# Performance work log

Hardware: AMD Instinct MI355X
Metric: run time of the kernel (lower is better)

Reference implementation:

```python
import jax, jax.numpy as jnp
import numpy as np

NUM_HEADS = 8
ATTN_C = 8
EPS = 1e-5


def setup_inputs() -> dict:
    key = jax.random.key(0)
    ks = jax.random.split(key, 8)
    B, S, R, C = 1, 2048, 384, 64
    H, c = NUM_HEADS, ATTN_C
    sc = 1.0 / np.sqrt(C)
    return {
        "x1d": jax.random.normal(ks[0], (B, S, R, C), dtype=jnp.float32),
        "ln_w": jnp.ones((C,), jnp.float32),
        "ln_b": jnp.zeros((C,), jnp.float32),
        "Wq": jax.random.normal(ks[1], (C, H * c), jnp.float32) * sc,
        "Wk": jax.random.normal(ks[2], (C, c), jnp.float32) * sc,
        "Wv": jax.random.normal(ks[3], (C, c), jnp.float32) * sc,
        "Wg": jax.random.normal(ks[4], (C, H * c), jnp.float32) * sc,
        "bg": jnp.zeros((H * c,), jnp.float32),
        "Wf": jax.random.normal(ks[5], (H * c, C), jnpp := jnp.float32) * sc,
        "bf": jnp.zeros((C,), jnp.float32),
    }


def reference(x1d, ln_w, ln_b, Wq, Wk, Wv, Wg, bg, Wf, bf):
    H, c = NUM_HEADS, ATTN_C
    # swap seq/res axes: [B, S, R, C] -> [B, R, S, C]; attention runs over S (MSA column)
    x = jnp.swapaxes(x1d, -2, -3)
    mu = jnp.mean(x, axis=-1, keepdims=True)
    var = jnp.mean(jnp.square(x - mu), axis=-1, keepdims=True)
    xn = (x - mu) / jnp.sqrt(var + EPS) * ln_w + ln_b
    B, R, S, C = xn.shape
    # mean-pooled query over the sequence axis
    q_avg = jnp.mean(xn, axis=-2)                                  # [B, R, C]
    q = (q_avg @ Wq).reshape(B, R, H, c) * (c ** -0.5)             # [B, R, H, c]
    k = xn @ Wk                                                    # [B, R, S, c] (single shared head)
    v = xn @ Wv                                                    # [B, R, S, c]
    gate = jax.nn.sigmoid((xn @ Wg + bg).reshape(B, R, S, H, c))   # [B, R, S, H, c]
    w = jax.nn.softmax(jnp.einsum('brhc,brsc->brhs', q, k), axis=-1)  # [B, R, H, S]
    o = jnp.einsum('brhs,brsc->brhc', w, v)                        # [B, R, H, c]
    out = (o[:, :, None, :, :] * gate).reshape(B, R, S, H * c)     # broadcast over S, gated
    out = out @ Wf + bf                                            # [B, R, S, C]
    return jnp.swapaxes(out, -2, -3)                               # [B, S, R, C]
```

## Files before the change

kernel.cpp:

```cpp
#include <hip/hip_runtime.h>

#define SEQ  2048
#define RDIM 384
#define CDIM 64

typedef __attribute__((ext_vector_type(8))) short s16x8;
typedef __attribute__((ext_vector_type(4))) float f32x4;
#define MFMA(a,b,c) __builtin_amdgcn_mfma_f32_16x16x32_bf16(a,b,c,0,0,0)

__device__ __forceinline__ unsigned short f2bf(float x) {
    union { float f; unsigned u; } a; a.f = x;
    unsigned r = a.u + 0x7fffu + ((a.u >> 16) & 1u);
    return (unsigned short)(r >> 16);
}
__device__ __forceinline__ float bf2f(unsigned u16) {
    union { unsigned u; float f; } a; a.u = u16 << 16; return a.f;
}
__device__ __forceinline__ float sigmoidf_(float z) { return 1.0f / (1.0f + __expf(-z)); }

#define SWZ(row,k) ((row)*64 + (((((k)>>3) ^ ((row)&7)))<<3) + ((k)&7))

__global__ __launch_bounds__(256) void k_prep(
    const float* __restrict__ Wk, const float* __restrict__ Wv,
    const float* __restrict__ Wg, const float* __restrict__ Wf,
    unsigned short* __restrict__ wkvt, unsigned short* __restrict__ wgt,
    unsigned short* __restrict__ wfp)
{
    const int t = threadIdx.x, b = blockIdx.x;
    if (b == 0) {
        for (int idx = t; idx < 16 * 64; idx += 256) {
            const int kc = idx >> 6, k = idx & 63;
            const float v = (kc < 8) ? Wk[k * 8 + kc] : Wv[k * 8 + (kc - 8)];
            wkvt[SWZ(kc, k)] = f2bf(v);
        }
    } else if (b == 1) {
        for (int idx = t; idx < 64 * 64; idx += 256) {
            const int col = idx >> 6, k = idx & 63;
            wgt[SWZ(col, k)] = f2bf(Wg[k * 64 + col]);
        }
    } else {
        for (int idx = t; idx < 64 * 64; idx += 256) {
            const int cout = idx >> 6, p = idx & 63;
            const int kst = p >> 5, h = (p >> 3) & 3, rr = p & 7;
            const int j = kst * 32 + (rr < 4 ? 4 * h + rr : 16 + 4 * h + (rr - 4));
            wfp[SWZ(cout, p)] = f2bf(Wf[j * 64 + cout]);
        }
    }
}

__global__ __launch_bounds__(256) void k_phase1(
    const float* __restrict__ x, const float* __restrict__ lnw, const float* __restrict__ lnb,
    const unsigned short* __restrict__ wkvt,
    float* __restrict__ qpart, unsigned short* __restrict__ kv)
{
    __shared__ __align__(16) unsigned short xs[128 * 64];
    __shared__ __align__(16) unsigned short wkv[16 * 64];
    const int t = threadIdx.x;
    ((unsigned*)wkv)[t]       = ((const unsigned*)wkvt)[t];
    ((unsigned*)wkv)[t + 256] = ((const unsigned*)wkvt)[t + 256];

    const int rtile  = blockIdx.x % 24;
    const int schunk = blockIdx.x / 24;
    const int g  = t >> 4;
    const int c4 = t & 15;
    const int r  = rtile * 16 + g;
    const int wv = t >> 6, lane = t & 63, hi = lane >> 4, l15 = lane & 15;
    const float4 lw = *(const float4*)(lnw + (c4 << 2));
    const float4 lb = *(const float4*)(lnb + (c4 << 2));

    float qs0 = 0.f, qs1 = 0.f, qs2 = 0.f, qs3 = 0.f;
    for (int sub = 0; sub < 8; ++sub) {
        __syncthreads();
        #pragma unroll
        for (int it = 0; it < 8; ++it) {
            const int row = it * 16 + g;
            const int s = schunk * 64 + sub * 8 + it;
            const float4 xv = *(const float4*)(x + ((size_t)s * RDIM + r) * CDIM + (c4 << 2));
            float sum = xv.x + xv.y + xv.z + xv.w;
            float sq  = xv.x * xv.x + xv.y * xv.y + xv.z * xv.z + xv.w * xv.w;
            #pragma unroll
            for (int m = 1; m < 16; m <<= 1) {
                sum += __shfl_xor(sum, m, 16);
                sq  += __shfl_xor(sq,  m, 16);
            }
            const float mu   = sum * (1.0f / 64.0f);
            const float rstd = rsqrtf(sq * (1.0f / 64.0f) - mu * mu + 1e-5f);
            const float xn0 = (xv.x - mu) * rstd * lw.x + lb.x;
            const float xn1 = (xv.y - mu) * rstd * lw.y + lb.y;
            const float xn2 = (xv.z - mu) * rstd * lw.z + lb.z;
            const float xn3 = (xv.w - mu) * rstd * lw.w + lb.w;
            qs0 += xn0; qs1 += xn1; qs2 += xn2; qs3 += xn3;
            ushort4 pk; pk.x = f2bf(xn0); pk.y = f2bf(xn1); pk.z = f2bf(xn2); pk.w = f2bf(xn3);
            *(ushort4*)&xs[row * 64 + ((((c4 >> 1) ^ (row & 7)) << 3) | ((c4 & 1) << 2))] = pk;
        }
        __syncthreads();
        f32x4 acc0 = 0, acc1 = 0;
        #pragma unroll
        for (int kst = 0; kst < 2; ++kst) {
            const int kg = (kst * 4 + hi);
            const s16x8 a = *(const s16x8*)&wkv[l15 * 64 + ((kg ^ (l15 & 7)) << 3)];
            const int row0 = wv * 32 + l15;
            const s16x8 b0 = *(const s16x8*)&xs[row0 * 64 + ((kg ^ (l15 & 7)) << 3)];
            const s16x8 b1 = *(const s16x8*)&xs[(row0 + 16) * 64 + ((kg ^ (l15 & 7)) << 3)];
            acc0 = MFMA(a, b0, acc0);
            acc1 = MFMA(a, b1, acc1);
        }
        #pragma unroll
        for (int ni = 0; ni < 2; ++ni) {
            const f32x4 av = ni ? acc1 : acc0;
            const int srow = schunk * 64 + sub * 8 + 2 * wv + ni;
            const int rrow = rtile * 16 + l15;
            ushort4 pk; pk.x = f2bf(av[0]); pk.y = f2bf(av[1]); pk.z = f2bf(av[2]); pk.w = f2bf(av[3]);
            *(ushort4*)(kv + ((size_t)srow * RDIM + rrow) * 16 + (hi << 2)) = pk;
        }
    }
    float4 q4; q4.x = qs0; q4.y = qs1; q4.z = qs2; q4.w = qs3;
    *(float4*)(qpart + ((size_t)schunk * RDIM + r) * CDIM + (c4 << 2)) = q4;
}

__global__ __launch_bounds__(256) void k_phase2(
    const float* __restrict__ qpart, const float* __restrict__ Wq,
    const unsigned short* __restrict__ kv, float* __restrict__ obuf)
{
    __shared__ float qa[64];
    __shared__ float ql[64];
    __shared__ float hredm[4][8];
    __shared__ float hredd[4][8];
    __shared__ float maxs[8];
    __shared__ float dens[8];
    __shared__ float wred[4][64];
    const int t = threadIdx.x;
    const int r = (blockIdx.x & 7) * 48 + (blockIdx.x >> 3);
    if (t < 64) {
        float ssum = 0.f;
        #pragma unroll
        for (int ch = 0; ch < 32; ch++) ssum += qpart[(size_t)ch * (RDIM * CDIM) + r * 64 + t];
        qa[t] = ssum;
    }
    __syncthreads();
    if (t < 64) {
        float a = 0.f;
        for (int i = 0; i < 64; i++) a += qa[i] * Wq[i * 64 + t];
        ql[t] = a * (1.0f / 2048.0f) * 0.35355339059327373f;
    }
    __syncthreads();

    const unsigned short* kvr = kv + (size_t)r * 16;
    float l[8][8];
    #pragma unroll
    for (int i = 0; i < 8; i++) {
        const int s = t + i * 256;
        const uint4 ku = *(const uint4*)(kvr + (size_t)s * (RDIM * 16));
        float kf[8];
        kf[0] = bf2f(ku.x & 0xffff); kf[1] = bf2f(ku.x >> 16);
        kf[2] = bf2f(ku.y & 0xffff); kf[3] = bf2f(ku.y >> 16);
        kf[4] = bf2f(ku.z & 0xffff); kf[5] = bf2f(ku.z >> 16);
        kf[6] = bf2f(ku.w & 0xffff); kf[7] = bf2f(ku.w >> 16);
        #pragma unroll
        for (int h = 0; h < 8; h++) {
            float a = 0.f;
            #pragma unroll
            for (int c = 0; c < 8; c++) a += ql[h * 8 + c] * kf[c];
            l[i][h] = a;
        }
    }
    float pm[8];
    #pragma unroll
    for (int h = 0; h < 8; h++) {
        pm[h] = l[0][h];
        #pragma unroll
        for (int i = 1; i < 8; i++) pm[h] = fmaxf(pm[h], l[i][h]);
    }
    #pragma unroll
    for (int m = 1; m < 64; m <<= 1) {
        #pragma unroll
        for (int h = 0; h < 8; h++) pm[h] = fmaxf(pm[h], __shfl_xor(pm[h], m, 64));
    }
    const int wvi = t >> 6, lane = t & 63;
    if (lane == 0) {
        #pragma unroll
        for (int h = 0; h < 8; h++) hredm[wvi][h] = pm[h];
    }
    __syncthreads();
    if (t < 8) maxs[t] = fmaxf(fmaxf(hredm[0][t], hredm[1][t]), fmaxf(hredm[2][t], hredm[3][t]));
    __syncthreads();

    float pd[8] = {0,0,0,0,0,0,0,0};
    #pragma unroll
    for (int i = 0; i < 8; i++) {
        #pragma unroll
        for (int h = 0; h < 8; h++) {
            const float e = __expf(l[i][h] - maxs[h]);
            l[i][h] = e;
            pd[h] += e;
        }
    }
    #pragma unroll
    for (int m = 1; m < 64; m <<= 1) {
        #pragma unroll
        for (int h = 0; h < 8; h++) pd[h] += __shfl_xor(pd[h], m, 64);
    }
    if (lane == 0) {
        #pragma unroll
        for (int h = 0; h < 8; h++) hredd[wvi][h] = pd[h];
    }
    __syncthreads();
    if (t < 8) dens[t] = hredd[0][t] + hredd[1][t] + hredd[2][t] + hredd[3][t];

    float acc[64];
    #pragma unroll
    for (int j = 0; j < 64; j++) acc[j] = 0.f;
    #pragma unroll
    for (int i = 0; i < 8; i++) {
        const int s = t + i * 256;
        const uint4 vu = *(const uint4*)(kvr + (size_t)s * (RDIM * 16) + 8);
        float vf[8];
        vf[0] = bf2f(vu.x & 0xffff); vf[1] = bf2f(vu.x >> 16);
        vf[2] = bf2f(vu.y & 0xffff); vf[3] = bf2f(vu.y >> 16);
        vf[4] = bf2f(vu.z & 0xffff); vf[5] = bf2f(vu.z >> 16);
        vf[6] = bf2f(vu.w & 0xffff); vf[7] = bf2f(vu.w >> 16);
        #pragma unroll
        for (int h = 0; h < 8; h++) {
            const float w = l[i][h];
            #pragma unroll
            for (int c = 0; c < 8; c++) acc[h * 8 + c] += w * vf[c];
        }
    }
    #pragma unroll
    for (int m = 1; m < 64; m <<= 1) {
        #pragma unroll
        for (int j = 0; j < 64; j++) acc[j] += __shfl_xor(acc[j], m, 64);
    }
    if (lane == 0) {
        #pragma unroll
        for (int j = 0; j < 64; j++) wred[wvi][j] = acc[j];
    }
    __syncthreads();
    if (t < 64)
        obuf[(size_t)r * 64 + t] = (wred[0][t] + wred[1][t] + wred[2][t] + wred[3][t]) / dens[t >> 3];
}

__global__ __launch_bounds__(256) void k_phase3(
    const float* __restrict__ x, const float* __restrict__ lnw, const float* __restrict__ lnb,
    const unsigned short* __restrict__ wgt, const unsigned short* __restrict__ wfp,
    const float* __restrict__ bg, const float* __restrict__ bf_,
    const float* __restrict__ obuf, float* __restrict__ out)
{
    __shared__ __align__(16) unsigned short xs[128 * 64];
    __shared__ __align__(16) unsigned short wg[64 * 64];
    __shared__ __align__(16) unsigned short wf[64 * 64];
    __shared__ __align__(16) unsigned short olds[128 * 68];
    __shared__ __align__(16) float bgl[64];
    __shared__ __align__(16) float bfl[64];
    const int t = threadIdx.x;
    const int rtile = blockIdx.x % 3;
    const int sb    = blockIdx.x / 3;
    const int rbase = rtile * 128;

    #pragma unroll
    for (int i = 0; i < 8; ++i) ((unsigned*)wg)[t + i * 256] = ((const unsigned*)wgt)[t + i * 256];
    #pragma unroll
    for (int i = 0; i < 8; ++i) ((unsigned*)wf)[t + i * 256] = ((const unsigned*)wfp)[t + i * 256];
    if (t < 64) { bgl[t] = bg[t]; bfl[t] = bf_[t]; }
    #pragma unroll
    for (int i = 0; i < 8; ++i) {
        const int idx = t + i * 256;
        const int row = idx >> 4, c = idx & 15;
        const float4 ov = *(const float4*)(obuf + (size_t)(rbase + row) * 64 + (c << 2));
        ushort4 pk; pk.x = f2bf(ov.x); pk.y = f2bf(ov.y); pk.z = f2bf(ov.z); pk.w = f2bf(ov.w);
        *(ushort4*)&olds[row * 68 + (c << 2)] = pk;
    }

    const int g = t >> 4, c4 = t & 15;
    const float4 lw = *(const float4*)(lnw + (c4 << 2));
    const float4 lb = *(const float4*)(lnb + (c4 << 2));
    const int wv = t >> 6, lane = t & 63, hi = lane >> 4, l15 = lane & 15;
    float bfv[4];

    for (int si = 0; si < 4; ++si) {
        const int s = sb * 4 + si;
        __syncthreads();
        #pragma unroll
        for (int it = 0; it < 8; ++it) {
            const int row = it * 16 + g;
            const float4 xv = *(const float4*)(x + ((size_t)s * RDIM + rbase + row) * CDIM + (c4 << 2));
            float sum = xv.x + xv.y + xv.z + xv.w;
            float sq  = xv.x * xv.x + xv.y * xv.y + xv.z * xv.z + xv.w * xv.w;
            #pragma unroll
            for (int m = 1; m < 16; m <<= 1) {
                sum += __shfl_xor(sum, m, 16);
                sq  += __shfl_xor(sq,  m, 16);
            }
            const float mu   = sum * (1.0f / 64.0f);
            const float rstd = rsqrtf(sq * (1.0f / 64.0f) - mu * mu + 1e-5f);
            ushort4 pk;
            pk.x = f2bf((xv.x - mu) * rstd * lw.x + lb.x);
            pk.y = f2bf((xv.y - mu) * rstd * lw.y + lb.y);
            pk.z = f2bf((xv.z - mu) * rstd * lw.z + lb.z);
            pk.w = f2bf((xv.w - mu) * rstd * lw.w + lb.w);
            *(ushort4*)&xs[row * 64 + ((((c4 >> 1) ^ (row & 7)) << 3) | ((c4 & 1) << 2))] = pk;
        }
        __syncthreads();

        f32x4 acc1[4][2];
        #pragma unroll
        for (int mi = 0; mi < 4; ++mi) { acc1[mi][0] = 0; acc1[mi][1] = 0; }
        #pragma unroll
        for (int kst = 0; kst < 2; ++kst) {
            const int kg = kst * 4 + hi;
            s16x8 bfr[2];
            #pragma unroll
            for (int ni = 0; ni < 2; ++ni) {
                const int row = wv * 32 + ni * 16 + l15;
                bfr[ni] = *(const s16x8*)&xs[row * 64 + ((kg ^ (l15 & 7)) << 3)];
            }
            #pragma unroll
            for (int mi = 0; mi < 4; ++mi) {
                const int col = mi * 16 + l15;
                const s16x8 afr = *(const s16x8*)&wg[col * 64 + ((kg ^ (l15 & 7)) << 3)];
                acc1[mi][0] = MFMA(afr, bfr[0], acc1[mi][0]);
                acc1[mi][1] = MFMA(afr, bfr[1], acc1[mi][1]);
            }
        }

        s16x8 a2[2][2];
        #pragma unroll
        for (int ni = 0; ni < 2; ++ni) {
            const int row = wv * 32 + ni * 16 + l15;
            #pragma unroll
            for (int mi = 0; mi < 4; ++mi) {
                const int jb = mi * 16 + (hi << 2);
                const ushort4 ou = *(const ushort4*)&olds[row * 68 + jb];
                float o4[4];
                o4[0] = bf2f(ou.x); o4[1] = bf2f(ou.y); o4[2] = bf2f(ou.z); o4[3] = bf2f(ou.w);
                const f32x4 bg4 = *(const f32x4*)&bgl[jb];
                #pragma unroll
                for (int rg = 0; rg < 4; ++rg) {
                    const float z = acc1[mi][ni][rg] + bg4[rg];
                    const float tv = sigmoidf_(z) * o4[rg];
                    a2[ni][mi >> 1][((mi & 1) << 2) + rg] = (short)f2bf(tv);
                }
            }
        }

        f32x4 acc2[2][4];
        #pragma unroll
        for (int ni = 0; ni < 2; ++ni)
            #pragma unroll
            for (int ci = 0; ci < 4; ++ci) acc2[ni][ci] = 0;
        #pragma unroll
        for (int kst = 0; kst < 2; ++kst) {
            const int kg = kst * 4 + hi;
            #pragma unroll
            for (int ci = 0; ci < 4; ++ci) {
                const int co = ci * 16 + l15;
                const s16x8 bfr = *(const s16x8*)&wf[co * 64 + ((kg ^ (l15 & 7)) << 3)];
                acc2[0][ci] = MFMA(a2[0][kst], bfr, acc2[0][ci]);
                acc2[1][ci] = MFMA(a2[1][kst], bfr, acc2[1][ci]);
            }
        }

        #pragma unroll
        for (int ci = 0; ci < 4; ++ci) bfv[ci] = bfl[ci * 16 + l15];
        #pragma unroll
        for (int ni = 0; ni < 2; ++ni) {
            #pragma unroll
            for (int rg = 0; rg < 4; ++rg) {
                const int row = wv * 32 + ni * 16 + (hi << 2) + rg;
                float* op = out + ((size_t)s * RDIM + rbase + row) * CDIM + l15;
                #pragma unroll
                for (int ci = 0; ci < 4; ++ci)
                    op[ci * 16] = acc2[ni][ci][rg] + bfv[ci];
            }
        }
    }
}

extern "C" void kernel_launch(void* const* d_in, const int* in_sizes, int n_in,
                              void* d_out, int out_size, void* d_ws, size_t ws_size,
                              hipStream_t stream)
{
    const float* x   = (const float*)d_in[0];
    const float* lnw = (const float*)d_in[1];
    const float* lnb = (const float*)d_in[2];
    const float* Wq  = (const float*)d_in[3];
    const float* Wk  = (const float*)d_in[4];
    const float* Wv  = (const float*)d_in[5];
    const float* Wg  = (const float*)d_in[6];
    const float* bg  = (const float*)d_in[7];
    const float* Wf  = (const float*)d_in[8];
    const float* bf  = (const float*)d_in[9];

    char* ws = (char*)d_ws;
    float* qpart         = (float*)ws;
    float* obuf          = (float*)(ws + 3145728);
    unsigned short* kv   = (unsigned short*)(ws + 3244032);
    unsigned short* wkvt = (unsigned short*)(ws + 28409856);
    unsigned short* wgt  = wkvt + 1024;
    unsigned short* wfp  = wgt + 4096;

    float* outp = (float*)d_out;

    k_prep<<<3, 256, 0, stream>>>(Wk, Wv, Wg, Wf, wkvt, wgt, wfp);
    k_phase1<<<768, 256, 0, stream>>>(x, lnw, lnb, wkvt, qpart, kv);
    k_phase2<<<384, 256, 0, stream>>>(qpart, Wq, kv, obuf);
    k_phase3<<<1536, 256, 0, stream>>>(x, lnw, lnb, wgt, wfp, bg, bf, obuf, outp);
}
```

Baseline: 181.3 us.

## Fold LayerNorm affine into weights, split softmax phase, double-buffer gating kernel

Folds the LayerNorm scale and shift into the K/V, gate and query weights, with precomputed bias vectors, so the per-element affine work disappears from phase 1 and phase 3. Moves kv to a residue-major layout and rewrites phase 2 as a single-pass softmax without max subtraction, split over two sequence halves, plus a small combine kernel. That kernel also writes the attention output pre-swizzled into the phase 3 register fragment layout. Phase 3 processes 8 sequence rows per block with register prefetch of the next row, double-buffered LDS, float4 output stores and launch bounds for 3 blocks per CU. Dropping the max subtraction risks exp overflow if logits become large.

```diff
diff --git a/kernel.cpp b/kernel.cpp
--- a/kernel.cpp
+++ b/kernel.cpp
@@ -13,30 +13,49 @@
     unsigned r = a.u + 0x7fffu + ((a.u >> 16) & 1u);
     return (unsigned short)(r >> 16);
 }
+__device__ __forceinline__ unsigned pack2(float lo, float hi) {
+    return (unsigned)f2bf(lo) | ((unsigned)f2bf(hi) << 16);
+}
 __device__ __forceinline__ float bf2f(unsigned u16) {
     union { unsigned u; float f; } a; a.u = u16 << 16; return a.f;
 }
-__device__ __forceinline__ float sigmoidf_(float z) { return 1.0f / (1.0f + __expf(-z)); }
+__device__ __forceinline__ float uaf(unsigned u) {
+    union { unsigned u; float f; } a; a.u = u; return a.f;
+}
 
 #define SWZ(row,k) ((row)*64 + (((((k)>>3) ^ ((row)&7)))<<3) + ((k)&7))
 
 __global__ __launch_bounds__(256) void k_prep(
     const float* __restrict__ Wk, const float* __restrict__ Wv,
     const float* __restrict__ Wg, const float* __restrict__ Wf,
+    const float* __restrict__ lnw, const float* __restrict__ lnb,
+    const float* __restrict__ bg,
     unsigned short* __restrict__ wkvt, unsigned short* __restrict__ wgt,
-    unsigned short* __restrict__ wfp)
+    unsigned short* __restrict__ wfp, float* __restrict__ kvbias,
+    float* __restrict__ bgp)
 {
     const int t = threadIdx.x, b = blockIdx.x;
     if (b == 0) {
         for (int idx = t; idx < 16 * 64; idx += 256) {
             const int kc = idx >> 6, k = idx & 63;
-            const float v = (kc < 8) ? Wk[k * 8 + kc] : Wv[k * 8 + (kc - 8)];
+            const float v = lnw[k] * ((kc < 8) ? Wk[k * 8 + kc] : Wv[k * 8 + (kc - 8)]);
             wkvt[SWZ(kc, k)] = f2bf(v);
+        }
+        if (t < 16) {
+            float a = 0.f;
+            for (int k = 0; k < 64; k++)
+                a += lnb[k] * ((t < 8) ? Wk[k * 8 + t] : Wv[k * 8 + (t - 8)]);
+            kvbias[t] = a;
         }
     } else if (b == 1) {
         for (int idx = t; idx < 64 * 64; idx += 256) {
             const int col = idx >> 6, k = idx & 63;
-            wgt[SWZ(col, k)] = f2bf(Wg[k * 64 + col]);
+            wgt[SWZ(col, k)] = f2bf(lnw[k] * Wg[k * 64 + col]);
+        }
+        if (t < 64) {
+            float a = bg[t];
+            for (int k = 0; k < 64; k++) a += lnb[k] * Wg[k * 64 + t];
+            bgp[t] = a;
         }
     } else {
         for (int idx = t; idx < 64 * 64; idx += 256) {
@@ -49,8 +68,7 @@
 }
 
 __global__ __launch_bounds__(256) void k_phase1(
-    const float* __restrict__ x, const float* __restrict__ lnw, const float* __restrict__ lnb,
-    const unsigned short* __restrict__ wkvt,
+    const float* __restrict__ x, const unsigned short* __restrict__ wkvt,
     float* __restrict__ qpart, unsigned short* __restrict__ kv)
 {
     __shared__ __align__(16) unsigned short xs[128 * 64];
@@ -63,10 +81,8 @@
     const int schunk = blockIdx.x / 24;
     const int g  = t >> 4;
     const int c4 = t & 15;
-    const int r  = rtile * 16 + g;
+    const int r = rtile * 16 + g;
     const int wv = t >> 6, lane = t & 63, hi = lane >> 4, l15 = lane & 15;
-    const float4 lw = *(const float4*)(lnw + (c4 << 2));
-    const float4 lb = *(const float4*)(lnb + (c4 << 2));
 
     float qs0 = 0.f, qs1 = 0.f, qs2 = 0.f, qs3 = 0.f;
     for (int sub = 0; sub < 8; ++sub) {
@@ -85,10 +101,10 @@
             }
             const float mu   = sum * (1.0f / 64.0f);
             const float rstd = rsqrtf(sq * (1.0f / 64.0f) - mu * mu + 1e-5f);
-            const float xn0 = (xv.x - mu) * rstd * lw.x + lb.x;
-            const float xn1 = (xv.y - mu) * rstd * lw.y + lb.y;
-            const float xn2 = (xv.z - mu) * rstd * lw.z + lb.z;
-            const float xn3 = (xv.w - mu) * rstd * lw.w + lb.w;
+            const float xn0 = (xv.x - mu) * rstd;
+            const float xn1 = (xv.y - mu) * rstd;
+            const float xn2 = (xv.z - mu) * rstd;
+            const float xn3 = (xv.w - mu) * rstd;
             qs0 += xn0; qs1 += xn1; qs2 += xn2; qs3 += xn3;
             ushort4 pk; pk.x = f2bf(xn0); pk.y = f2bf(xn1); pk.z = f2bf(xn2); pk.w = f2bf(xn3);
             *(ushort4*)&xs[row * 64 + ((((c4 >> 1) ^ (row & 7)) << 3) | ((c4 & 1) << 2))] = pk;
@@ -111,26 +127,27 @@
             const int srow = schunk * 64 + sub * 8 + 2 * wv + ni;
             const int rrow = rtile * 16 + l15;
             ushort4 pk; pk.x = f2bf(av[0]); pk.y = f2bf(av[1]); pk.z = f2bf(av[2]); pk.w = f2bf(av[3]);
-            *(ushort4*)(kv + ((size_t)srow * RDIM + rrow) * 16 + (hi << 2)) = pk;
+            *(ushort4*)(kv + ((size_t)rrow * SEQ + srow) * 16 + (hi << 2)) = pk;
         }
     }
     float4 q4; q4.x = qs0; q4.y = qs1; q4.z = qs2; q4.w = qs3;
     *(float4*)(qpart + ((size_t)schunk * RDIM + r) * CDIM + (c4 << 2)) = q4;
 }
 
-__global__ __launch_bounds__(256) void k_phase2(
+__global__ __launch_bounds__(256) void k_phase2a(
     const float* __restrict__ qpart, const float* __restrict__ Wq,
-    const unsigned short* __restrict__ kv, float* __restrict__ obuf)
+    const float* __restrict__ lnw, const float* __restrict__ lnb,
+    const float* __restrict__ kvbias, const unsigned short* __restrict__ kv,
+    float* __restrict__ num, float* __restrict__ den)
 {
     __shared__ float qa[64];
     __shared__ float ql[64];
-    __shared__ float hredm[4][8];
+    __shared__ float lbias[8];
     __shared__ float hredd[4][8];
-    __shared__ float maxs[8];
-    __shared__ float dens[8];
     __shared__ float wred[4][64];
     const int t = threadIdx.x;
-    const int r = (blockIdx.x & 7) * 48 + (blockIdx.x >> 3);
+    const int r = blockIdx.x >> 1;
+    const int half = blockIdx.x & 1;
     if (t < 64) {
         float ssum = 0.f;
         #pragma unroll
@@ -140,209 +157,208 @@
     __syncthreads();
     if (t < 64) {
         float a = 0.f;
-        for (int i = 0; i < 64; i++) a += qa[i] * Wq[i * 64 + t];
-        ql[t] = a * (1.0f / 2048.0f) * 0.35355339059327373f;
+        for (int i = 0; i < 64; i++)
+            a += (qa[i] * (1.0f / 2048.0f) * lnw[i] + lnb[i]) * Wq[i * 64 + t];
+        ql[t] = a * 0.35355339059327373f;
     }
     __syncthreads();
-
-    const unsigned short* kvr = kv + (size_t)r * 16;
-    float l[8][8];
-    #pragma unroll
-    for (int i = 0; i < 8; i++) {
-        const int s = t + i * 256;
-        const uint4 ku = *(const uint4*)(kvr + (size_t)s * (RDIM * 16));
-        float kf[8];
+    if (t < 8) {
+        float a = 0.f;
+        #pragma unroll
+        for (int c = 0; c < 8; c++) a += ql[t * 8 + c] * kvbias[c];
+        lbias[t] = a;
+    }
+    __syncthreads();
+
+    const unsigned short* kvr = kv + (size_t)r * (SEQ * 16);
+    float acc[64];
+    float pd[8];
+    #pragma unroll
+    for (int j = 0; j < 64; j++) acc[j] = 0.f;
+    #pragma unroll
+    for (int h = 0; h < 8; h++) pd[h] = 0.f;
+
+    #pragma unroll
+    for (int i = 0; i < 4; i++) {
+        const int s = half * 1024 + i * 256 + t;
+        const uint4 ku = *(const uint4*)(kvr + (size_t)s * 16);
+        const uint4 vu = *(const uint4*)(kvr + (size_t)s * 16 + 8);
+        float kf[8], vf[8];
         kf[0] = bf2f(ku.x & 0xffff); kf[1] = bf2f(ku.x >> 16);
         kf[2] = bf2f(ku.y & 0xffff); kf[3] = bf2f(ku.y >> 16);
         kf[4] = bf2f(ku.z & 0xffff); kf[5] = bf2f(ku.z >> 16);
         kf[6] = bf2f(ku.w & 0xffff); kf[7] = bf2f(ku.w >> 16);
-        #pragma unroll
-        for (int h = 0; h < 8; h++) {
-            float a = 0.f;
-            #pragma unroll
-            for (int c = 0; c < 8; c++) a += ql[h * 8 + c] * kf[c];
-            l[i][h] = a;
-        }
-    }
-    float pm[8];
-    #pragma unroll
-    for (int h = 0; h < 8; h++) {
-        pm[h] = l[0][h];
-        #pragma unroll
-        for (int i = 1; i < 8; i++) pm[h] = fmaxf(pm[h], l[i][h]);
-    }
-    #pragma unroll
-    for (int m = 1; m < 64; m <<= 1) {
-        #pragma unroll
-        for (int h = 0; h < 8; h++) pm[h] = fmaxf(pm[h], __shfl_xor(pm[h], m, 64));
-    }
-    const int wvi = t >> 6, lane = t & 63;
-    if (lane == 0) {
-        #pragma unroll
-        for (int h = 0; h < 8; h++) hredm[wvi][h] = pm[h];
-    }
-    __syncthreads();
-    if (t < 8) maxs[t] = fmaxf(fmaxf(hredm[0][t], hredm[1][t]), fmaxf(hredm[2][t], hredm[3][t]));
-    __syncthreads();
-
-    float pd[8] = {0,0,0,0,0,0,0,0};
-    #pragma unroll
-    for (int i = 0; i < 8; i++) {
-        #pragma unroll
-        for (int h = 0; h < 8; h++) {
-            const float e = __expf(l[i][h] - maxs[h]);
-            l[i][h] = e;
-            pd[h] += e;
-        }
-    }
-    #pragma unroll
-    for (int m = 1; m < 64; m <<= 1) {
-        #pragma unroll
-        for (int h = 0; h < 8; h++) pd[h] += __shfl_xor(pd[h], m, 64);
-    }
-    if (lane == 0) {
-        #pragma unroll
-        for (int h = 0; h < 8; h++) hredd[wvi][h] = pd[h];
-    }
-    __syncthreads();
-    if (t < 8) dens[t] = hredd[0][t] + hredd[1][t] + hredd[2][t] + hredd[3][t];
-
-    float acc[64];
-    #pragma unroll
-    for (int j = 0; j < 64; j++) acc[j] = 0.f;
-    #pragma unroll
-    for (int i = 0; i < 8; i++) {
-        const int s = t + i * 256;
-        const uint4 vu = *(const uint4*)(kvr + (size_t)s * (RDIM * 16) + 8);
-        float vf[8];
         vf[0] = bf2f(vu.x & 0xffff); vf[1] = bf2f(vu.x >> 16);
         vf[2] = bf2f(vu.y & 0xffff); vf[3] = bf2f(vu.y >> 16);
         vf[4] = bf2f(vu.z & 0xffff); vf[5] = bf2f(vu.z >> 16);
         vf[6] = bf2f(vu.w & 0xffff); vf[7] = bf2f(vu.w >> 16);
         #pragma unroll
         for (int h = 0; h < 8; h++) {
-            const float w = l[i][h];
-            #pragma unroll
-            for (int c = 0; c < 8; c++) acc[h * 8 + c] += w * vf[c];
+            float a = lbias[h];
+            #pragma unroll
+            for (int c = 0; c < 8; c++) a += ql[h * 8 + c] * kf[c];
+            const float e = __expf(a);
+            pd[h] += e;
+            #pragma unroll
+            for (int c = 0; c < 8; c++) acc[h * 8 + c] += e * vf[c];
         }
     }
     #pragma unroll
     for (int m = 1; m < 64; m <<= 1) {
         #pragma unroll
         for (int j = 0; j < 64; j++) acc[j] += __shfl_xor(acc[j], m, 64);
-    }
+        #pragma unroll
+        for (int h = 0; h < 8; h++) pd[h] += __shfl_xor(pd[h], m, 64);
+    }
+    const int wvi = t >> 6, lane = t & 63;
     if (lane == 0) {
         #pragma unroll
         for (int j = 0; j < 64; j++) wred[wvi][j] = acc[j];
+        #pragma unroll
+        for (int h = 0; h < 8; h++) hredd[wvi][h] = pd[h];
     }
     __syncthreads();
     if (t < 64)
-        obuf[(size_t)r * 64 + t] = (wred[0][t] + wred[1][t] + wred[2][t] + wred[3][t]) / dens[t >> 3];
-}
-
-__global__ __launch_bounds__(256) void k_phase3(
-    const float* __restrict__ x, const float* __restrict__ lnw, const float* __restrict__ lnb,
+        num[(size_t)(half * RDIM + r) * 64 + t] = wred[0][t] + wred[1][t] + wred[2][t] + wred[3][t];
+    if (t < 8)
+        den[(size_t)(half * RDIM + r) * 8 + t] = hredd[0][t] + hredd[1][t] + hredd[2][t] + hredd[3][t];
+}
+
+__global__ __launch_bounds__(256) void k_phase2b(
+    const float* __restrict__ num, const float* __restrict__ den,
+    const float* __restrict__ kvbias, unsigned short* __restrict__ ofimg)
+{
+    const int idx = blockIdx.x * 256 + threadIdx.x;
+    const int r = idx >> 6, c = idx & 63;
+    const float n = num[idx] + num[RDIM * 64 + idx];
+    const float d = den[r * 8 + (c >> 3)] + den[(RDIM + r) * 8 + (c >> 3)];
+    const float o = n / d + kvbias[8 + (c & 7)];
+    const int rt = r >> 7, row = r & 127;
+    const int wv = row >> 5, ni = (row >> 4) & 1, l15 = row & 15;
+    const int mi = c >> 4, hi = (c >> 2) & 3, rg = c & 3;
+    const int tt = wv * 64 + hi * 16 + l15;
+    const int slot = ni * 16 + mi * 4 + rg;
+    ofimg[((rt * 256 + tt) << 5) + slot] = f2bf(o);
+}
+
+__global__ __launch_bounds__(256, 3) void k_phase3(
+    const float* __restrict__ x,
     const unsigned short* __restrict__ wgt, const unsigned short* __restrict__ wfp,
-    const float* __restrict__ bg, const float* __restrict__ bf_,
-    const float* __restrict__ obuf, float* __restrict__ out)
-{
-    __shared__ __align__(16) unsigned short xs[128 * 64];
+    const float* __restrict__ bgp, const float* __restrict__ bf_,
+    const unsigned short* __restrict__ ofimg, float* __restrict__ out)
+{
+    __shared__ __align__(16) unsigned short xs[2][128 * 64];
     __shared__ __align__(16) unsigned short wg[64 * 64];
     __shared__ __align__(16) unsigned short wf[64 * 64];
-    __shared__ __align__(16) unsigned short olds[128 * 68];
-    __shared__ __align__(16) float bgl[64];
-    __shared__ __align__(16) float bfl[64];
     const int t = threadIdx.x;
-    const int rtile = blockIdx.x % 3;
-    const int sb    = blockIdx.x / 3;
-    const int rbase = rtile * 128;
+    const int rt = blockIdx.x % 3;
+    const int sb = blockIdx.x / 3;
+    const int rbase = rt * 128;
 
     #pragma unroll
     for (int i = 0; i < 8; ++i) ((unsigned*)wg)[t + i * 256] = ((const unsigned*)wgt)[t + i * 256];
     #pragma unroll
     for (int i = 0; i < 8; ++i) ((unsigned*)wf)[t + i * 256] = ((const unsigned*)wfp)[t + i * 256];
-    if (t < 64) { bgl[t] = bg[t]; bfl[t] = bf_[t]; }
-    #pragma unroll
-    for (int i = 0; i < 8; ++i) {
-        const int idx = t + i * 256;
-        const int row = idx >> 4, c = idx & 15;
-        const float4 ov = *(const float4*)(obuf + (size_t)(rbase + row) * 64 + (c << 2));
-        ushort4 pk; pk.x = f2bf(ov.x); pk.y = f2bf(ov.y); pk.z = f2bf(ov.z); pk.w = f2bf(ov.w);
-        *(ushort4*)&olds[row * 68 + (c << 2)] = pk;
-    }
-
-    const int g = t >> 4, c4 = t & 15;
-    const float4 lw = *(const float4*)(lnw + (c4 << 2));
-    const float4 lb = *(const float4*)(lnb + (c4 << 2));
+
     const int wv = t >> 6, lane = t & 63, hi = lane >> 4, l15 = lane & 15;
-    float bfv[4];
-
-    for (int si = 0; si < 4; ++si) {
-        const int s = sb * 4 + si;
-        __syncthreads();
-        #pragma unroll
-        for (int it = 0; it < 8; ++it) {
-            const int row = it * 16 + g;
-            const float4 xv = *(const float4*)(x + ((size_t)s * RDIM + rbase + row) * CDIM + (c4 << 2));
-            float sum = xv.x + xv.y + xv.z + xv.w;
-            float sq  = xv.x * xv.x + xv.y * xv.y + xv.z * xv.z + xv.w * xv.w;
-            #pragma unroll
-            for (int m = 1; m < 16; m <<= 1) {
-                sum += __shfl_xor(sum, m, 16);
-                sq  += __shfl_xor(sq,  m, 16);
-            }
+
+    unsigned opk[16];
+    {
+        const unsigned* osrc = (const unsigned*)ofimg + (size_t)(rt * 256 + t) * 16;
+        #pragma unroll
+        for (int i = 0; i < 16; ++i) opk[i] = osrc[i];
+    }
+    float bgf[4][4], bff[4][4];
+    #pragma unroll
+    for (int mi = 0; mi < 4; ++mi) *(float4*)bgf[mi] = *(const float4*)(bgp + mi * 16 + hi * 4);
+    #pragma unroll
+    for (int ci = 0; ci < 4; ++ci) *(float4*)bff[ci] = *(const float4*)(bf_ + ci * 16 + hi * 4);
+
+    const int li = t & 3, p = t >> 2;
+    float4 xv[2][4];
+    {
+        const int s0 = sb * 8;
+        #pragma unroll
+        for (int k = 0; k < 2; ++k) {
+            const float* xp = x + ((size_t)s0 * RDIM + rbase + k * 64 + p) * CDIM + li * 16;
+            #pragma unroll
+            for (int j = 0; j < 4; ++j) xv[k][j] = *(const float4*)(xp + j * 4);
+        }
+    }
+
+    for (int si = 0; si < 8; ++si) {
+        const int s = sb * 8 + si;
+        unsigned short* xb = xs[si & 1];
+        #pragma unroll
+        for (int k = 0; k < 2; ++k) {
+            const int row = k * 64 + p;
+            float sum = 0.f, sq = 0.f;
+            #pragma unroll
+            for (int j = 0; j < 4; ++j) {
+                sum += xv[k][j].x + xv[k][j].y + xv[k][j].z + xv[k][j].w;
+                sq  += xv[k][j].x * xv[k][j].x + xv[k][j].y * xv[k][j].y
+                     + xv[k][j].z * xv[k][j].z + xv[k][j].w * xv[k][j].w;
+            }
+            sum += __shfl_xor(sum, 1, 4); sum += __shfl_xor(sum, 2, 4);
+            sq  += __shfl_xor(sq,  1, 4); sq  += __shfl_xor(sq,  2, 4);
             const float mu   = sum * (1.0f / 64.0f);
             const float rstd = rsqrtf(sq * (1.0f / 64.0f) - mu * mu + 1e-5f);
-            ushort4 pk;
-            pk.x = f2bf((xv.x - mu) * rstd * lw.x + lb.x);
-            pk.y = f2bf((xv.y - mu) * rstd * lw.y + lb.y);
-            pk.z = f2bf((xv.z - mu) * rstd * lw.z + lb.z);
-            pk.w = f2bf((xv.w - mu) * rstd * lw.w + lb.w);
-            *(ushort4*)&xs[row * 64 + ((((c4 >> 1) ^ (row & 7)) << 3) | ((c4 & 1) << 2))] = pk;
-        }
-        __syncthreads();
+            uint4 w0, w1;
+            w0.x = pack2((xv[k][0].x - mu) * rstd, (xv[k][0].y - mu) * rstd);
+            w0.y = pack2((xv[k][0].z - mu) * rstd, (xv[k][0].w - mu) * rstd);
+            w0.z = pack2((xv[k][1].x - mu) * rstd, (xv[k][1].y - mu) * rstd);
+            w0.w = pack2((xv[k][1].z - mu) * rstd, (xv[k][1].w - mu) * rstd);
+            w1.x = pack2((xv[k][2].x - mu) * rstd, (xv[k][2].y - mu) * rstd);
+            w1.y = pack2((xv[k][2].z - mu) * rstd, (xv[k][2].w - mu) * rstd);
+            w1.z = pack2((xv[k][3].x - mu) * rstd, (xv[k][3].y - mu) * rstd);
+            w1.w = pack2((xv[k][3].z - mu) * rstd, (xv[k][3].w - mu) * rstd);
+            *(uint4*)&xb[row * 64 + (((2 * li)     ^ (row & 7)) << 3)] = w0;
+            *(uint4*)&xb[row * 64 + (((2 * li + 1) ^ (row & 7)) << 3)] = w1;
+        }
+        if (si < 7) {
+            const int sn = s + 1;
+            #pragma unroll
+            for (int k = 0; k < 2; ++k) {
+                const float* xp = x + ((size_t)sn * RDIM + rbase + k * 64 + p) * CDIM + li * 16;
+                #pragma unroll
+                for (int j = 0; j < 4; ++j) xv[k][j] = *(const float4*)(xp + j * 4);
+            }
+        }
+        asm volatile("s_waitcnt lgkmcnt(0)" ::: "memory");
+        __builtin_amdgcn_s_barrier();
+        asm volatile("" ::: "memory");
 
         f32x4 acc1[4][2];
         #pragma unroll
         for (int mi = 0; mi < 4; ++mi) { acc1[mi][0] = 0; acc1[mi][1] = 0; }
         #pragma unroll
         for (int kst = 0; kst < 2; ++kst) {
-            const int kg = kst * 4 + hi;
-            s16x8 bfr[2];
-            #pragma unroll
-            for (int ni = 0; ni < 2; ++ni) {
-                const int row = wv * 32 + ni * 16 + l15;
-                bfr[ni] = *(const s16x8*)&xs[row * 64 + ((kg ^ (l15 & 7)) << 3)];
-            }
+            const int swz = (((kst * 4 + hi) ^ (l15 & 7)) << 3);
+            const s16x8 bfr0 = *(const s16x8*)&xb[(wv * 32 + l15) * 64 + swz];
+            const s16x8 bfr1 = *(const s16x8*)&xb[(wv * 32 + 16 + l15) * 64 + swz];
             #pragma unroll
             for (int mi = 0; mi < 4; ++mi) {
-                const int col = mi * 16 + l15;
-                const s16x8 afr = *(const s16x8*)&wg[col * 64 + ((kg ^ (l15 & 7)) << 3)];
-                acc1[mi][0] = MFMA(afr, bfr[0], acc1[mi][0]);
-                acc1[mi][1] = MFMA(afr, bfr[1], acc1[mi][1]);
-            }
-        }
-
+                const s16x8 afr = *(const s16x8*)&wg[(mi * 16 + l15) * 64 + swz];
+                acc1[mi][0] = MFMA(afr, bfr0, acc1[mi][0]);
+                acc1[mi][1] = MFMA(afr, bfr1, acc1[mi][1]);
+            }
+        }
         s16x8 a2[2][2];
         #pragma unroll
         for (int ni = 0; ni < 2; ++ni) {
-            const int row = wv * 32 + ni * 16 + l15;
             #pragma unroll
             for (int mi = 0; mi < 4; ++mi) {
-                const int jb = mi * 16 + (hi << 2);
-                const ushort4 ou = *(const ushort4*)&olds[row * 68 + jb];
-                float o4[4];
-                o4[0] = bf2f(ou.x); o4[1] = bf2f(ou.y); o4[2] = bf2f(ou.z); o4[3] = bf2f(ou.w);
-                const f32x4 bg4 = *(const f32x4*)&bgl[jb];
                 #pragma unroll
                 for (int rg = 0; rg < 4; ++rg) {
-                    const float z = acc1[mi][ni][rg] + bg4[rg];
-                    const float tv = sigmoidf_(z) * o4[rg];
+                    const int slot = ni * 16 + mi * 4 + rg;
+                    const unsigned u = opk[slot >> 1];
+                    const float of = uaf((slot & 1) ? (u & 0xffff0000u) : (u << 16));
+                    const float z = acc1[mi][ni][rg] + bgf[mi][rg];
+                    const float tv = of / (1.0f + __expf(-z));
                     a2[ni][mi >> 1][((mi & 1) << 2) + rg] = (short)f2bf(tv);
                 }
             }
         }
-
         f32x4 acc2[2][4];
         #pragma unroll
         for (int ni = 0; ni < 2; ++ni)
@@ -350,27 +366,25 @@
             for (int ci = 0; ci < 4; ++ci) acc2[ni][ci] = 0;
         #pragma unroll
         for (int kst = 0; kst < 2; ++kst) {
-            const int kg = kst * 4 + hi;
+            const int swz = (((kst * 4 + hi) ^ (l15 & 7)) << 3);
             #pragma unroll
             for (int ci = 0; ci < 4; ++ci) {
-                const int co = ci * 16 + l15;
-                const s16x8 bfr = *(const s16x8*)&wf[co * 64 + ((kg ^ (l15 & 7)) << 3)];
-                acc2[0][ci] = MFMA(a2[0][kst], bfr, acc2[0][ci]);
-                acc2[1][ci] = MFMA(a2[1][kst], bfr, acc2[1][ci]);
-            }
-        }
-
-        #pragma unroll
-        for (int ci = 0; ci < 4; ++ci) bfv[ci] = bfl[ci * 16 + l15];
+                const s16x8 wffr = *(const s16x8*)&wf[(ci * 16 + l15) * 64 + swz];
+                acc2[0][ci] = MFMA(wffr, a2[0][kst], acc2[0][ci]);
+                acc2[1][ci] = MFMA(wffr, a2[1][kst], acc2[1][ci]);
+            }
+        }
         #pragma unroll
         for (int ni = 0; ni < 2; ++ni) {
-            #pragma unroll
-            for (int rg = 0; rg < 4; ++rg) {
-                const int row = wv * 32 + ni * 16 + (hi << 2) + rg;
-                float* op = out + ((size_t)s * RDIM + rbase + row) * CDIM + l15;
-                #pragma unroll
-                for (int ci = 0; ci < 4; ++ci)
-                    op[ci * 16] = acc2[ni][ci][rg] + bfv[ci];
+            float* op = out + ((size_t)s * RDIM + rbase + wv * 32 + ni * 16 + l15) * 64 + hi * 4;
+            #pragma unroll
+            for (int ci = 0; ci < 4; ++ci) {
+                float4 res;
+                res.x = acc2[ni][ci][0] + bff[ci][0];
+                res.y = acc2[ni][ci][1] + bff[ci][1];
+                res.z = acc2[ni][ci][2] + bff[ci][2];
+                res.w = acc2[ni][ci][3] + bff[ci][3];
+                *(float4*)(op + ci * 16) = res;
             }
         }
     }
@@ -392,17 +406,22 @@
     const float* bf  = (const float*)d_in[9];
 
     char* ws = (char*)d_ws;
-    float* qpart         = (float*)ws;
-    float* obuf          = (float*)(ws + 3145728);
-    unsigned short* kv   = (unsigned short*)(ws + 3244032);
-    unsigned short* wkvt = (unsigned short*)(ws + 28409856);
-    unsigned short* wgt  = wkvt + 1024;
-    unsigned short* wfp  = wgt + 4096;
+    float*          qpart  = (float*)ws;
+    unsigned short* kv     = (unsigned short*)(ws + 3145728);
+    float*          num    = (float*)(ws + 28311552);
+    float*          den    = (float*)(ws + 28508160);
+    unsigned short* ofimg  = (unsigned short*)(ws + 28532736);
+    unsigned short* wkvt   = (unsigned short*)(ws + 28581888);
+    unsigned short* wgt    = (unsigned short*)(ws + 28583936);
+    unsigned short* wfp    = (unsigned short*)(ws + 28592128);
+    float*          kvbias = (float*)(ws + 28600320);
+    float*          bgp    = (float*)(ws + 28600384);
 
     float* outp = (float*)d_out;
 
-    k_prep<<<3, 256, 0, stream>>>(Wk, Wv, Wg, Wf, wkvt, wgt, wfp);
-    k_phase1<<<768, 256, 0, stream>>>(x, lnw, lnb, wkvt, qpart, kv);
-    k_phase2<<<384, 256, 0, stream>>>(qpart, Wq, kv, obuf);
-    k_phase3<<<1536, 256, 0, stream>>>(x, lnw, lnb, wgt, wfp, bg, bf, obuf, outp);
-}
+    k_prep<<<3, 256, 0, stream>>>(Wk, Wv, Wg, Wf, lnw, lnb, bg, wkvt, wgt, wfp, kvbias, bgp);
+    k_phase1<<<768, 256, 0, stream>>>(x, wkvt, qpart, kv);
+    k_phase2a<<<768, 256, 0, stream>>>(qpart, Wq, lnw, lnb, kvbias, kv, num, den);
+    k_phase2b<<<96, 256, 0, stream>>>(num, den, kvbias, ofimg);
+    k_phase3<<<768, 256, 0, stream>>>(x, wgt, wfp, bgp, bf, ofimg, outp);
+}
```

After: 171.6 us, median of 2. -5.4%, faster.
